# Kernel optimization log

Measured on AMD Instinct MI355X. Metric: run time of the kernel, lower is better.

The kernel has to match this reference:

```python
import jax, jax.numpy as jnp
import numpy as np

# Dimensions: state [N, d, n, 2] with last axis = (q, p)
N, D, NN = 256, 8, 32
FEAT = D * NN          # flattened q features = 256
HID = 256              # MLP hidden width
DT = 0.01              # integration step
STEPS = 100            # number of RK4 steps (sequential)


def setup_inputs() -> dict:
    key = jax.random.key(0)
    k0, k1, k2 = jax.random.split(key, 3)
    x0 = 0.1 * jax.random.normal(k0, (N, D, NN, 2), dtype=jnp.float32)
    W1 = jax.random.normal(k1, (FEAT, HID), dtype=jnp.float32) / np.float32(np.sqrt(FEAT))
    b1 = jnp.zeros((HID,), dtype=jnp.float32)
    W2 = jax.random.normal(k2, (HID, 1), dtype=jnp.float32) / np.float32(np.sqrt(HID))
    b2 = jnp.zeros((1,), dtype=jnp.float32)
    return {"x0": x0, "W1": W1, "b1": b1, "W2": W2, "b2": b2}


def _hamiltonian(x, W1, b1, W2, b2):
    # x: [N, d, n, 2] -> H: [N]
    q = x[..., 0]
    p = x[..., 1]
    kinetic = 0.5 * jnp.sum(p * p, axis=(1, 2))          # [N]
    qf = q.reshape(q.shape[0], -1)                        # [N, d*n]
    h = jnp.tanh(qf @ W1 + b1)                            # [N, HID]
    V = (h @ W2 + b2)[:, 0]                               # [N]
    return kinetic + V


def _vector_field(x, params):
    # Hamiltonian vector field: dq/dt = dH/dp, dp/dt = -dH/dq (t-independent)
    g = jax.grad(lambda xx: jnp.sum(_hamiltonian(xx, *params)))(x)  # [N,d,n,2]
    return jnp.stack([g[..., 1], -g[..., 0]], axis=-1)


def _rk4_step(x, eps, params):
    k1 = _vector_field(x, params)
    k2 = _vector_field(x + 0.5 * eps * k1, params)
    k3 = _vector_field(x + 0.5 * eps * k2, params)
    k4 = _vector_field(x + eps * k3, params)
    return x + (eps / 6.0) * (k1 + 2.0 * k2 + 2.0 * k3 + k4)


def reference(x0, W1, b1, W2, b2):
    params = (W1, b1, W2, b2)
    eps = jnp.float32(DT)

    def step(x, _):
        return _rk4_step(x, eps, params), None

    xT, _ = jax.lax.scan(step, x0, None, length=STEPS)
    return xT
```

## Files before the change

kernel.cpp:

```cpp
#include <hip/hip_runtime.h>
#include <stdint.h>


typedef _Float16 v8h __attribute__((ext_vector_type(8)));
typedef float v4f __attribute__((ext_vector_type(4)));

#define NFULL 12
#define WS 264
#define US 272

#define MFMA_AV(C, A, B) \
    asm("v_mfma_f32_16x16x32_f16 %0, %1, %2, %0" : "+v"(C) : "v"(A), "a"(B))

__device__ __forceinline__ float bfly4(float x) {
    float a = x, b = x;
    asm("v_permlane16_swap_b32 %0, %1" : "+v"(a), "+v"(b));
    float s = a + b;
    float c = s, d = s;
    asm("v_permlane32_swap_b32 %0, %1" : "+v"(c), "+v"(d));
    return c + d;
}

__device__ __forceinline__ float ueval2(float zz, float w4) {
    float e_ = __expf(zz);
    float r_ = __builtin_amdgcn_rcpf(e_ + 1.f);
    return w4 * __builtin_fmaf(-r_, r_, r_);
}

__global__ __launch_bounds__(1024, 4)
void ham_kernel(const float* __restrict__ x0, const float* __restrict__ W1,
                const float* __restrict__ b1, const float* __restrict__ W2,
                float* __restrict__ out)
{
    __shared__ __align__(16)  _Float16 wldsT[256 * WS];
    __shared__ __align__(128) char     upool[20480];
    float*    mscr = (float*)upool;
    _Float16* ubuf = (_Float16*)upool;

    const int t = threadIdx.x;
    const int w = t >> 6;
    const int l = t & 63;
    const int quad = l >> 4;
    const int s = l & 15;
    const int c0 = 16 * w + s;
    const int blk = blockIdx.x;
    const int sel = (s & 3) * US;

    {
        const int c = t & 255;
        const int rbase = (t >> 8) * 64;
        #pragma unroll 1
        for (int r0 = 0; r0 < 64; r0 += 8) {
            v8h h;
            #pragma unroll
            for (int j = 0; j < 8; ++j)
                h[j] = (_Float16)W1[(rbase + r0 + j) * 256 + c];
            *(v8h*)(wldsT + c * WS + rbase + r0) = h;
        }
    }
    __syncthreads();

    v8h wF0[8];
    #pragma unroll
    for (int kk = 0; kk < 8; ++kk)
        wF0[kk] = *(const v8h*)(wldsT + c0 * WS + 32 * kk + 8 * quad);

    v8h wM0[8];
    float* scr0 = mscr + w * 320;
    #pragma unroll
    for (int kb = 0; kb < 16; ++kb) {
        v8h aM[8];
        #pragma unroll
        for (int kk = 0; kk < 8; ++kk)
            aM[kk] = *(const v8h*)(wldsT + (16 * kb + s) * WS
                                          + 32 * kk + 8 * quad);
        v4f D0 = {0.f,0.f,0.f,0.f};
        #pragma unroll
        for (int kk = 0; kk < 8; ++kk)
            D0 = __builtin_amdgcn_mfma_f32_16x16x32_f16(aM[kk], wF0[kk], D0, 0, 0, 0);
        *(v4f*)(scr0 + s * 20 + 4 * quad) = D0;
        asm volatile("s_waitcnt lgkmcnt(0)" ::: "memory");
        if ((quad >> 1) == (kb & 1)) {
            #pragma unroll
            for (int j = 0; j < 8; ++j)
                wM0[kb >> 1][j] = (_Float16)scr0[s * 20 + 8 * (quad & 1) + j];
        }
        asm volatile("s_waitcnt lgkmcnt(0)" ::: "memory");
    }
    __syncthreads();

    const float b1r0 = b1[c0];
    const float w4 = 4.f * W2[c0];
    float2 qp0 = ((const float2*)(x0 + (size_t)blk * 512))[c0];
    const float q0o0 = qp0.x, p0o0 = qp0.y;

    if (quad == 0) {
        ubuf[c0] = (_Float16)q0o0;
        ubuf[US + c0] = (_Float16)p0o0;
        ubuf[2 * US + c0] = (_Float16)0.f;
        ubuf[3 * US + c0] = (_Float16)0.f;
    }
    __syncthreads();
    float z1, P;
    {
        const _Float16* ab = ubuf + sel + 8 * quad;
        v4f C0a = {0.f,0.f,0.f,0.f}, C0b = {0.f,0.f,0.f,0.f};
        #pragma unroll
        for (int kk = 0; kk < 8; kk += 2) {
            v8h a0 = *(const v8h*)(ab + 32 * kk);
            v8h a1 = *(const v8h*)(ab + 32 * (kk + 1));
            C0a = __builtin_amdgcn_mfma_f32_16x16x32_f16(a0, wF0[kk], C0a, 0, 0, 0);
            C0b = __builtin_amdgcn_mfma_f32_16x16x32_f16(a1, wF0[kk + 1], C0b, 0, 0, 0);
        }
        v4f C0s = C0a + C0b;
        z1 = C0s[0] + b1r0;  P = C0s[1];
    }
    __syncthreads();

    const float dt = 0.01f, hdt = 0.005f, dt6 = 0.01f / 6.f;
    const float dtdt6 = dt * dt6, hdt2 = hdt * hdt, dthdt = dt * hdt;
    const float K8dt = 8.f * dt, K4dt = 4.f * dt;
    const float j1 = 2.f * (float)quad, j2 = j1 + 1.f;
    const float cPn1 = -(j1 * 0.125f * dt6), cPn2 = -(j2 * 0.125f * dt6);
    const float Kz1a = 2.f * j1 * dt,        Kz1b = 2.f * j2 * dt;
    const float KB1 = dtdt6 * j1 * (8.f - j1) * 0.125f;
    const float KB2 = dtdt6 * j2 * (8.f - j2) * 0.125f;
    const float KVn1 = -(j1 * dtdt6 * 0.25f), KVn2 = -(j2 * dtdt6 * 0.25f);
    const float K2hdt = 2.f * hdt;
    const float K2dt  = 2.f * dt;
    const float KC1n = -(2.f * hdt2) / 3.f;
    const float KC2n = -(2.f * dthdt) / 3.f;
    const float w71 = 7.f - j1;
    const float w31 = 3.f - j1;

    const int cw = c0 ^ (quad << 3);
    const int R0 = 4 * quad;
    const int wo0 = (R0 + 0) * US + cw;
    const int wo1 = (R0 + 1) * US + (cw ^ 32);
    const int wo2 = (R0 + 2) * US + cw;
    const int wo3 = (R0 + 3) * US + (cw ^ 32);
    const int sx = (s >> 2) & 3;
    const int rbase = s * US + 8 * (quad ^ sx);
    const int sodd = (s & 1) << 5;
    const _Float16* pe = ubuf + rbase + sodd;
    const _Float16* po = ubuf + rbase + 32 - sodd;

    float SBp = 0.f, SVp = 0.f;
    float AL1 = 0.f, AL2 = 0.f;
    float S1p = 0.f, S23p = 0.f;
    float cn1 = 99.f - j1;

    #pragma unroll 1
    for (int e = 0; e < NFULL; ++e) {
        const int bo = (e & 1) * (16 * US);

        float z1d = z1 + z1;
        float Pp1  = __builtin_fmaf(cPn1, SBp, P);
        float zp21 = __builtin_fmaf(Kz1a, P, z1d);
        zp21 = __builtin_fmaf(KB1, SBp, zp21);
        zp21 = __builtin_fmaf(KVn1, SVp, zp21);
        float zb21 = __builtin_fmaf(K2hdt, Pp1, zp21);
        float zc21 = __builtin_fmaf(KC1n, AL1, zb21);
        float zd21 = __builtin_fmaf(K2dt, Pp1, zp21);
        zd21 = __builtin_fmaf(KC2n, AL1, zd21);
        float Pp2  = __builtin_fmaf(cPn2, SBp, P);
        float zp22 = __builtin_fmaf(Kz1b, P, z1d);
        zp22 = __builtin_fmaf(KB2, SBp, zp22);
        zp22 = __builtin_fmaf(KVn2, SVp, zp22);
        float zb22 = __builtin_fmaf(K2hdt, Pp2, zp22);
        float zc22 = __builtin_fmaf(KC1n, AL2, zb22);
        float zd22 = __builtin_fmaf(K2dt, Pp2, zp22);
        zd22 = __builtin_fmaf(KC2n, AL2, zd22);

        float ua1 = ueval2(zp21, w4), ub1 = ueval2(zb21, w4);
        float uc1 = ueval2(zc21, w4), ud1 = ueval2(zd21, w4);
        float ua2 = ueval2(zp22, w4), ub2 = ueval2(zb22, w4);
        float uc2 = ueval2(zc22, w4), ud2 = ueval2(zd22, w4);

        float tv1 = ub1 + uc1;
        float uA1 = ua1 + tv1;
        float uB1 = __builtin_fmaf(2.f, tv1, ua1 + ud1);
        float tv2 = ub2 + uc2;
        float uA2 = ua2 + tv2;
        float uB2 = __builtin_fmaf(2.f, tv2, ua2 + ud2);

        ubuf[bo + wo0] = (_Float16)uA1;
        ubuf[bo + wo1] = (_Float16)uB1;
        ubuf[bo + wo2] = (_Float16)uA2;
        ubuf[bo + wo3] = (_Float16)uB2;
        __syncthreads();

        v4f C0s;
        {
            v4f C0a = {0.f,0.f,0.f,0.f}, C0b = {0.f,0.f,0.f,0.f};
            #pragma unroll
            for (int kk = 0; kk < 8; kk += 2) {
                v8h a0 = *(const v8h*)(pe + bo + 32 * kk);
                v8h a1 = *(const v8h*)(po + bo + 32 * kk);
                MFMA_AV(C0a, a0, wM0[kk]);
                MFMA_AV(C0b, a1, wM0[kk + 1]);
            }
            C0s = C0a + C0b;
        }

        float A1 = C0s[0], B1 = C0s[1], A2 = C0s[2], B2 = C0s[3];
        float Bs = B1 + B2;
        float V  = __builtin_fmaf(w71, Bs, A1 + A2 - B2);
        float SB = bfly4(Bs);
        float SV = bfly4(V);

        z1 = __builtin_fmaf(K8dt, P, z1);
        z1 = __builtin_fmaf(-dtdt6, SV, z1);
        P  = __builtin_fmaf(-dt6, SB, P);

        SBp = SB;  SVp = SV;  AL1 = A1;  AL2 = A2;

        S1p += uB1 + uB2;
        S23p = __builtin_fmaf(cn1, uB1, S23p) + uA1;
        S23p = __builtin_fmaf(cn1 - 1.f, uB2, S23p) + uA2;
        cn1 -= 8.f;
    }

    {
        const float vm = (quad < 2) ? 1.f : 0.f;
        float z1d = z1 + z1;
        float Pp1  = __builtin_fmaf(cPn1, SBp, P);
        float zp21 = __builtin_fmaf(Kz1a, P, z1d);
        zp21 = __builtin_fmaf(KB1, SBp, zp21);
        zp21 = __builtin_fmaf(KVn1, SVp, zp21);
        float zb21 = __builtin_fmaf(K2hdt, Pp1, zp21);
        float zc21 = __builtin_fmaf(KC1n, AL1, zb21);
        float zd21 = __builtin_fmaf(K2dt, Pp1, zp21);
        zd21 = __builtin_fmaf(KC2n, AL1, zd21);
        float Pp2  = __builtin_fmaf(cPn2, SBp, P);
        float zp22 = __builtin_fmaf(Kz1b, P, z1d);
        zp22 = __builtin_fmaf(KB2, SBp, zp22);
        zp22 = __builtin_fmaf(KVn2, SVp, zp22);
        float zb22 = __builtin_fmaf(K2hdt, Pp2, zp22);
        float zc22 = __builtin_fmaf(KC1n, AL2, zb22);
        float zd22 = __builtin_fmaf(K2dt, Pp2, zp22);
        zd22 = __builtin_fmaf(KC2n, AL2, zd22);

        float ua1 = ueval2(zp21, w4), ub1 = ueval2(zb21, w4);
        float uc1 = ueval2(zc21, w4), ud1 = ueval2(zd21, w4);
        float ua2 = ueval2(zp22, w4), ub2 = ueval2(zb22, w4);
        float uc2 = ueval2(zc22, w4), ud2 = ueval2(zd22, w4);

        float tv1 = ub1 + uc1;
        float uA1 = (ua1 + tv1) * vm;
        float uB1 = __builtin_fmaf(2.f, tv1, ua1 + ud1) * vm;
        float tv2 = ub2 + uc2;
        float uA2 = (ua2 + tv2) * vm;
        float uB2 = __builtin_fmaf(2.f, tv2, ua2 + ud2) * vm;

        ubuf[wo0] = (_Float16)uA1;
        ubuf[wo1] = (_Float16)uB1;
        ubuf[wo2] = (_Float16)uA2;
        ubuf[wo3] = (_Float16)uB2;
        __syncthreads();

        v4f C0s;
        {
            v4f C0a = {0.f,0.f,0.f,0.f}, C0b = {0.f,0.f,0.f,0.f};
            #pragma unroll
            for (int kk = 0; kk < 8; kk += 2) {
                v8h a0 = *(const v8h*)(pe + 32 * kk);
                v8h a1 = *(const v8h*)(po + 32 * kk);
                MFMA_AV(C0a, a0, wM0[kk]);
                MFMA_AV(C0b, a1, wM0[kk + 1]);
            }
            C0s = C0a + C0b;
        }
        float A1 = C0s[0], B1 = C0s[1], A2 = C0s[2], B2 = C0s[3];
        float Bs = B1 + B2;
        float V  = __builtin_fmaf(w31, Bs, A1 + A2 - B2);
        float SB = bfly4(Bs);
        float SV = bfly4(V);
        z1 = __builtin_fmaf(K4dt, P, z1);
        z1 = __builtin_fmaf(-dtdt6, SV, z1);
        P  = __builtin_fmaf(-dt6, SB, P);
        S1p += uB1 + uB2;
        S23p = __builtin_fmaf(cn1, uB1, S23p) + uA1;
        S23p = __builtin_fmaf(cn1 - 1.f, uB2, S23p) + uA2;
    }

    const float S1f  = bfly4(S1p);
    const float S23f = bfly4(S23p);
    __syncthreads();
    if (quad == 0) {
        ubuf[c0] = (_Float16)S1f;
        ubuf[US + c0] = (_Float16)S23f;
        ubuf[2 * US + c0] = (_Float16)0.f;
        ubuf[3 * US + c0] = (_Float16)0.f;
    }
    __syncthreads();
    v8h wBt0[8];
    #pragma unroll
    for (int kk = 0; kk < 8; ++kk)
        #pragma unroll
        for (int j = 0; j < 8; ++j)
            wBt0[kk][j] = wldsT[(32 * kk + 8 * quad + j) * WS + c0];
    float D10, D20;
    {
        const _Float16* ab = ubuf + sel + 8 * quad;
        v4f C0a = {0.f,0.f,0.f,0.f}, C0b = {0.f,0.f,0.f,0.f};
        #pragma unroll
        for (int kk = 0; kk < 8; kk += 2) {
            v8h a0 = *(const v8h*)(ab + 32 * kk);
            v8h a1 = *(const v8h*)(ab + 32 * (kk + 1));
            C0a = __builtin_amdgcn_mfma_f32_16x16x32_f16(a0, wBt0[kk], C0a, 0, 0, 0);
            C0b = __builtin_amdgcn_mfma_f32_16x16x32_f16(a1, wBt0[kk + 1], C0b, 0, 0, 0);
        }
        v4f C0s = C0a + C0b;
        D10 = C0s[0];  D20 = C0s[1];
    }
    const float dt6e = 0.01f / 6.f, dtdt6e = 0.01f * dt6e;
    float pT0 = p0o0 - dt6e * D10;
    float qT0 = q0o0 + 0.01f * 100.f * p0o0 - dtdt6e * D20;

    if (quad == 0)
        ((float2*)(out + (size_t)blk * 512))[c0] = make_float2(qT0, pT0);
}

extern "C" void kernel_launch(void* const* d_in, const int* in_sizes, int n_in,
                              void* d_out, int out_size, void* d_ws, size_t ws_size,
                              hipStream_t stream) {
    const float* x0 = (const float*)d_in[0];
    const float* W1 = (const float*)d_in[1];
    const float* b1 = (const float*)d_in[2];
    const float* W2 = (const float*)d_in[3];
    float* out = (float*)d_out;
    hipLaunchKernelGGL(ham_kernel, dim3(256), dim3(1024), 0, stream,
                       x0, W1, b1, W2, out);
}
```

Before: 92.88 us.

## Process sixteen RK4 steps per barrier round with two MFMA chains

Result: slower. 98.32 us (+5.9%).

```diff
diff --git a/kernel.cpp b/kernel.cpp
--- a/kernel.cpp
+++ b/kernel.cpp
@@ -5,7 +5,7 @@
 typedef _Float16 v8h __attribute__((ext_vector_type(8)));
 typedef float v4f __attribute__((ext_vector_type(4)));
 
-#define NFULL 12
+#define NFULL 6
 #define WS 264
 #define US 272
 
@@ -27,15 +27,35 @@
     return w4 * __builtin_fmaf(-r_, r_, r_);
 }
 
+__device__ __forceinline__ void stage_eval(
+    float z1d, float P, float bb, float aa,
+    float KPn, float K2j, float KZBn, float KZAn, float AL,
+    float K2hdt, float K2dt, float KC1n, float KC2n, float w4,
+    float& uA, float& uB)
+{
+    float Pp  = __builtin_fmaf(KPn, bb, P);
+    float zp2 = __builtin_fmaf(K2j, P, z1d);
+    zp2 = __builtin_fmaf(KZBn, bb, zp2);
+    zp2 = __builtin_fmaf(KZAn, aa, zp2);
+    float zb2 = __builtin_fmaf(K2hdt, Pp, zp2);
+    float zc2 = __builtin_fmaf(KC1n, AL, zb2);
+    float zd2 = __builtin_fmaf(K2dt, Pp, zp2);
+    zd2 = __builtin_fmaf(KC2n, AL, zd2);
+    float ua = ueval2(zp2, w4), ub = ueval2(zb2, w4);
+    float uc = ueval2(zc2, w4), ud = ueval2(zd2, w4);
+    float tv = ub + uc;
+    uA = ua + tv;
+    uB = __builtin_fmaf(2.f, tv, ua + ud);
+}
+
 __global__ __launch_bounds__(1024, 4)
 void ham_kernel(const float* __restrict__ x0, const float* __restrict__ W1,
                 const float* __restrict__ b1, const float* __restrict__ W2,
                 float* __restrict__ out)
 {
-    __shared__ __align__(16)  _Float16 wldsT[256 * WS];
-    __shared__ __align__(128) char     upool[20480];
-    float*    mscr = (float*)upool;
-    _Float16* ubuf = (_Float16*)upool;
+    __shared__ __align__(128) _Float16 wldsT[256 * WS];
+    __shared__ __align__(16)  float    mscr[16 * 320];
+    _Float16* ubuf = wldsT;
 
     const int t = threadIdx.x;
     const int w = t >> 6;
@@ -44,6 +64,7 @@
     const int s = l & 15;
     const int c0 = 16 * w + s;
     const int blk = blockIdx.x;
+    const int kq = 8 * quad;
     const int sel = (s & 3) * US;
 
     {
@@ -63,7 +84,7 @@
     v8h wF0[8];
     #pragma unroll
     for (int kk = 0; kk < 8; ++kk)
-        wF0[kk] = *(const v8h*)(wldsT + c0 * WS + 32 * kk + 8 * quad);
+        wF0[kk] = *(const v8h*)(wldsT + c0 * WS + 32 * kk + kq);
 
     v8h wM0[8];
     float* scr0 = mscr + w * 320;
@@ -72,8 +93,7 @@
         v8h aM[8];
         #pragma unroll
         for (int kk = 0; kk < 8; ++kk)
-            aM[kk] = *(const v8h*)(wldsT + (16 * kb + s) * WS
-                                          + 32 * kk + 8 * quad);
+            aM[kk] = *(const v8h*)(wldsT + (16 * kb + s) * WS + 32 * kk + kq);
         v4f D0 = {0.f,0.f,0.f,0.f};
         #pragma unroll
         for (int kk = 0; kk < 8; ++kk)
@@ -103,7 +123,7 @@
     __syncthreads();
     float z1, P;
     {
-        const _Float16* ab = ubuf + sel + 8 * quad;
+        const _Float16* ab = ubuf + sel + kq;
         v4f C0a = {0.f,0.f,0.f,0.f}, C0b = {0.f,0.f,0.f,0.f};
         #pragma unroll
         for (int kk = 0; kk < 8; kk += 2) {
@@ -119,19 +139,22 @@
 
     const float dt = 0.01f, hdt = 0.005f, dt6 = 0.01f / 6.f;
     const float dtdt6 = dt * dt6, hdt2 = hdt * hdt, dthdt = dt * hdt;
-    const float K8dt = 8.f * dt, K4dt = 4.f * dt;
-    const float j1 = 2.f * (float)quad, j2 = j1 + 1.f;
-    const float cPn1 = -(j1 * 0.125f * dt6), cPn2 = -(j2 * 0.125f * dt6);
-    const float Kz1a = 2.f * j1 * dt,        Kz1b = 2.f * j2 * dt;
-    const float KB1 = dtdt6 * j1 * (8.f - j1) * 0.125f;
-    const float KB2 = dtdt6 * j2 * (8.f - j2) * 0.125f;
-    const float KVn1 = -(j1 * dtdt6 * 0.25f), KVn2 = -(j2 * dtdt6 * 0.25f);
-    const float K2hdt = 2.f * hdt;
-    const float K2dt  = 2.f * dt;
+    const float K16dt = 16.f * dt, K4dt = 4.f * dt;
+    const float K2hdt = 2.f * hdt, K2dt = 2.f * dt;
     const float KC1n = -(2.f * hdt2) / 3.f;
     const float KC2n = -(2.f * dthdt) / 3.f;
-    const float w71 = 7.f - j1;
-    const float w31 = 3.f - j1;
+    const float j1 = 2.f * (float)quad, j2 = j1 + 1.f;
+    const float j3 = j1 + 8.f,          j4 = j1 + 9.f;
+    const float KPn1 = -j1 * dt6, KPn2 = -j2 * dt6;
+    const float KPn3 = -j3 * dt6, KPn4 = -j4 * dt6;
+    const float K2j1 = 2.f * j1 * dt, K2j2 = 2.f * j2 * dt;
+    const float K2j3 = 2.f * j3 * dt, K2j4 = 2.f * j4 * dt;
+    const float KZB1 = -dtdt6 * j1 * (j1 - 1.f), KZB2 = -dtdt6 * j2 * (j2 - 1.f);
+    const float KZB3 = -dtdt6 * j3 * (j3 - 1.f), KZB4 = -dtdt6 * j4 * (j4 - 1.f);
+    const float KZA1 = -2.f * j1 * dtdt6, KZA2 = -2.f * j2 * dtdt6;
+    const float KZA3 = -2.f * j3 * dtdt6, KZA4 = -2.f * j4 * dtdt6;
+    const float w15 = 15.f - j1;
+    const float w3  = 3.f - j1;
 
     const int cw = c0 ^ (quad << 3);
     const int R0 = 4 * quad;
@@ -140,118 +163,94 @@
     const int wo2 = (R0 + 2) * US + cw;
     const int wo3 = (R0 + 3) * US + (cw ^ 32);
     const int sx = (s >> 2) & 3;
-    const int rbase = s * US + 8 * (quad ^ sx);
+    const int rbas = s * US + 8 * (quad ^ sx);
     const int sodd = (s & 1) << 5;
-    const _Float16* pe = ubuf + rbase + sodd;
-    const _Float16* po = ubuf + rbase + 32 - sodd;
-
-    float SBp = 0.f, SVp = 0.f;
-    float AL1 = 0.f, AL2 = 0.f;
+    const _Float16* pe = ubuf + rbas + sodd;
+    const _Float16* po = ubuf + rbas + 32 - sodd;
+
+    float bb = 0.f, aa = 0.f;
+    float AL1 = 0.f, AL2 = 0.f, AL3 = 0.f, AL4 = 0.f;
     float S1p = 0.f, S23p = 0.f;
-    float cn1 = 99.f - j1;
+    float cn = 99.f - j1;
 
     #pragma unroll 1
     for (int e = 0; e < NFULL; ++e) {
-        const int bo = (e & 1) * (16 * US);
+        const int bo = (e & 1) * (32 * US);
 
         float z1d = z1 + z1;
-        float Pp1  = __builtin_fmaf(cPn1, SBp, P);
-        float zp21 = __builtin_fmaf(Kz1a, P, z1d);
-        zp21 = __builtin_fmaf(KB1, SBp, zp21);
-        zp21 = __builtin_fmaf(KVn1, SVp, zp21);
-        float zb21 = __builtin_fmaf(K2hdt, Pp1, zp21);
-        float zc21 = __builtin_fmaf(KC1n, AL1, zb21);
-        float zd21 = __builtin_fmaf(K2dt, Pp1, zp21);
-        zd21 = __builtin_fmaf(KC2n, AL1, zd21);
-        float Pp2  = __builtin_fmaf(cPn2, SBp, P);
-        float zp22 = __builtin_fmaf(Kz1b, P, z1d);
-        zp22 = __builtin_fmaf(KB2, SBp, zp22);
-        zp22 = __builtin_fmaf(KVn2, SVp, zp22);
-        float zb22 = __builtin_fmaf(K2hdt, Pp2, zp22);
-        float zc22 = __builtin_fmaf(KC1n, AL2, zb22);
-        float zd22 = __builtin_fmaf(K2dt, Pp2, zp22);
-        zd22 = __builtin_fmaf(KC2n, AL2, zd22);
-
-        float ua1 = ueval2(zp21, w4), ub1 = ueval2(zb21, w4);
-        float uc1 = ueval2(zc21, w4), ud1 = ueval2(zd21, w4);
-        float ua2 = ueval2(zp22, w4), ub2 = ueval2(zb22, w4);
-        float uc2 = ueval2(zc22, w4), ud2 = ueval2(zd22, w4);
-
-        float tv1 = ub1 + uc1;
-        float uA1 = ua1 + tv1;
-        float uB1 = __builtin_fmaf(2.f, tv1, ua1 + ud1);
-        float tv2 = ub2 + uc2;
-        float uA2 = ua2 + tv2;
-        float uB2 = __builtin_fmaf(2.f, tv2, ua2 + ud2);
+        float uA1, uB1, uA2, uB2, uA3, uB3, uA4, uB4;
+        stage_eval(z1d, P, bb, aa, KPn1, K2j1, KZB1, KZA1, AL1,
+                   K2hdt, K2dt, KC1n, KC2n, w4, uA1, uB1);
+        stage_eval(z1d, P, bb, aa, KPn2, K2j2, KZB2, KZA2, AL2,
+                   K2hdt, K2dt, KC1n, KC2n, w4, uA2, uB2);
+        stage_eval(z1d, P, bb, aa, KPn3, K2j3, KZB3, KZA3, AL3,
+                   K2hdt, K2dt, KC1n, KC2n, w4, uA3, uB3);
+        stage_eval(z1d, P, bb, aa, KPn4, K2j4, KZB4, KZA4, AL4,
+                   K2hdt, K2dt, KC1n, KC2n, w4, uA4, uB4);
 
         ubuf[bo + wo0] = (_Float16)uA1;
         ubuf[bo + wo1] = (_Float16)uB1;
         ubuf[bo + wo2] = (_Float16)uA2;
         ubuf[bo + wo3] = (_Float16)uB2;
+        ubuf[bo + wo0 + 16 * US] = (_Float16)uA3;
+        ubuf[bo + wo1 + 16 * US] = (_Float16)uB3;
+        ubuf[bo + wo2 + 16 * US] = (_Float16)uA4;
+        ubuf[bo + wo3 + 16 * US] = (_Float16)uB4;
         __syncthreads();
 
-        v4f C0s;
+        v4f C0s, C1s;
         {
             v4f C0a = {0.f,0.f,0.f,0.f}, C0b = {0.f,0.f,0.f,0.f};
+            v4f C1a = {0.f,0.f,0.f,0.f}, C1b = {0.f,0.f,0.f,0.f};
             #pragma unroll
             for (int kk = 0; kk < 8; kk += 2) {
                 v8h a0 = *(const v8h*)(pe + bo + 32 * kk);
                 v8h a1 = *(const v8h*)(po + bo + 32 * kk);
+                v8h a2 = *(const v8h*)(pe + bo + 32 * kk + 16 * US);
+                v8h a3 = *(const v8h*)(po + bo + 32 * kk + 16 * US);
                 MFMA_AV(C0a, a0, wM0[kk]);
+                MFMA_AV(C1a, a2, wM0[kk]);
                 MFMA_AV(C0b, a1, wM0[kk + 1]);
+                MFMA_AV(C1b, a3, wM0[kk + 1]);
             }
-            C0s = C0a + C0b;
+            C0s = C0a + C0b;  C1s = C1a + C1b;
         }
 
         float A1 = C0s[0], B1 = C0s[1], A2 = C0s[2], B2 = C0s[3];
-        float Bs = B1 + B2;
-        float V  = __builtin_fmaf(w71, Bs, A1 + A2 - B2);
+        float A3 = C1s[0], B3 = C1s[1], A4 = C1s[2], B4 = C1s[3];
+        float Bs = (B1 + B2) + (B3 + B4);
+        float tV = (A1 + A2) + (A3 + A4) - B2;
+        tV = __builtin_fmaf(-8.f, B3, tV);
+        tV = __builtin_fmaf(-9.f, B4, tV);
+        float V  = __builtin_fmaf(w15, Bs, tV);
         float SB = bfly4(Bs);
         float SV = bfly4(V);
 
-        z1 = __builtin_fmaf(K8dt, P, z1);
+        z1 = __builtin_fmaf(K16dt, P, z1);
         z1 = __builtin_fmaf(-dtdt6, SV, z1);
         P  = __builtin_fmaf(-dt6, SB, P);
 
-        SBp = SB;  SVp = SV;  AL1 = A1;  AL2 = A2;
-
-        S1p += uB1 + uB2;
-        S23p = __builtin_fmaf(cn1, uB1, S23p) + uA1;
-        S23p = __builtin_fmaf(cn1 - 1.f, uB2, S23p) + uA2;
-        cn1 -= 8.f;
+        bb = SB * 0.0625f;
+        aa = __builtin_fmaf(-7.5f, SB, SV) * 0.0625f;
+        AL1 = A1;  AL2 = A2;  AL3 = A3;  AL4 = A4;
+
+        S1p += (uB1 + uB2) + (uB3 + uB4);
+        S23p = __builtin_fmaf(cn, uB1, S23p) + uA1;
+        S23p = __builtin_fmaf(cn - 1.f, uB2, S23p) + uA2;
+        S23p = __builtin_fmaf(cn - 8.f, uB3, S23p) + uA3;
+        S23p = __builtin_fmaf(cn - 9.f, uB4, S23p) + uA4;
+        cn -= 16.f;
     }
 
     {
         const float vm = (quad < 2) ? 1.f : 0.f;
         float z1d = z1 + z1;
-        float Pp1  = __builtin_fmaf(cPn1, SBp, P);
-        float zp21 = __builtin_fmaf(Kz1a, P, z1d);
-        zp21 = __builtin_fmaf(KB1, SBp, zp21);
-        zp21 = __builtin_fmaf(KVn1, SVp, zp21);
-        float zb21 = __builtin_fmaf(K2hdt, Pp1, zp21);
-        float zc21 = __builtin_fmaf(KC1n, AL1, zb21);
-        float zd21 = __builtin_fmaf(K2dt, Pp1, zp21);
-        zd21 = __builtin_fmaf(KC2n, AL1, zd21);
-        float Pp2  = __builtin_fmaf(cPn2, SBp, P);
-        float zp22 = __builtin_fmaf(Kz1b, P, z1d);
-        zp22 = __builtin_fmaf(KB2, SBp, zp22);
-        zp22 = __builtin_fmaf(KVn2, SVp, zp22);
-        float zb22 = __builtin_fmaf(K2hdt, Pp2, zp22);
-        float zc22 = __builtin_fmaf(KC1n, AL2, zb22);
-        float zd22 = __builtin_fmaf(K2dt, Pp2, zp22);
-        zd22 = __builtin_fmaf(KC2n, AL2, zd22);
-
-        float ua1 = ueval2(zp21, w4), ub1 = ueval2(zb21, w4);
-        float uc1 = ueval2(zc21, w4), ud1 = ueval2(zd21, w4);
-        float ua2 = ueval2(zp22, w4), ub2 = ueval2(zb22, w4);
-        float uc2 = ueval2(zc22, w4), ud2 = ueval2(zd22, w4);
-
-        float tv1 = ub1 + uc1;
-        float uA1 = (ua1 + tv1) * vm;
-        float uB1 = __builtin_fmaf(2.f, tv1, ua1 + ud1) * vm;
-        float tv2 = ub2 + uc2;
-        float uA2 = (ua2 + tv2) * vm;
-        float uB2 = __builtin_fmaf(2.f, tv2, ua2 + ud2) * vm;
+        float uA1, uB1, uA2, uB2;
+        stage_eval(z1d, P, bb, aa, KPn1, K2j1, KZB1, KZA1, AL1,
+                   K2hdt, K2dt, KC1n, KC2n, w4, uA1, uB1);
+        stage_eval(z1d, P, bb, aa, KPn2, K2j2, KZB2, KZA2, AL2,
+                   K2hdt, K2dt, KC1n, KC2n, w4, uA2, uB2);
+        uA1 *= vm;  uB1 *= vm;  uA2 *= vm;  uB2 *= vm;
 
         ubuf[wo0] = (_Float16)uA1;
         ubuf[wo1] = (_Float16)uB1;
@@ -273,15 +272,15 @@
         }
         float A1 = C0s[0], B1 = C0s[1], A2 = C0s[2], B2 = C0s[3];
         float Bs = B1 + B2;
-        float V  = __builtin_fmaf(w31, Bs, A1 + A2 - B2);
+        float V  = __builtin_fmaf(w3, Bs, A1 + A2 - B2);
         float SB = bfly4(Bs);
         float SV = bfly4(V);
         z1 = __builtin_fmaf(K4dt, P, z1);
         z1 = __builtin_fmaf(-dtdt6, SV, z1);
         P  = __builtin_fmaf(-dt6, SB, P);
         S1p += uB1 + uB2;
-        S23p = __builtin_fmaf(cn1, uB1, S23p) + uA1;
-        S23p = __builtin_fmaf(cn1 - 1.f, uB2, S23p) + uA2;
+        S23p = __builtin_fmaf(cn, uB1, S23p) + uA1;
+        S23p = __builtin_fmaf(cn - 1.f, uB2, S23p) + uA2;
     }
 
     const float S1f  = bfly4(S1p);
@@ -296,13 +295,20 @@
     __syncthreads();
     v8h wBt0[8];
     #pragma unroll
-    for (int kk = 0; kk < 8; ++kk)
-        #pragma unroll
-        for (int j = 0; j < 8; ++j)
-            wBt0[kk][j] = wldsT[(32 * kk + 8 * quad + j) * WS + c0];
+    for (int kk = 0; kk < 8; ++kk) {
+        const float* wp = W1 + c0 * 256 + 32 * kk + kq;
+        v4f lo = *(const v4f*)(wp);
+        v4f hi = *(const v4f*)(wp + 4);
+        v8h h;
+        h[0] = (_Float16)lo[0]; h[1] = (_Float16)lo[1];
+        h[2] = (_Float16)lo[2]; h[3] = (_Float16)lo[3];
+        h[4] = (_Float16)hi[0]; h[5] = (_Float16)hi[1];
+        h[6] = (_Float16)hi[2]; h[7] = (_Float16)hi[3];
+        wBt0[kk] = h;
+    }
     float D10, D20;
     {
-        const _Float16* ab = ubuf + sel + 8 * quad;
+        const _Float16* ab = ubuf + sel + kq;
         v4f C0a = {0.f,0.f,0.f,0.f}, C0b = {0.f,0.f,0.f,0.f};
         #pragma unroll
         for (int kk = 0; kk < 8; kk += 2) {
```
